# Optimization experiments

Measured on AMD Instinct MI355X. Metric: run time of the kernel, lower is better.

## Reference

```python
import math
import jax, jax.numpy as jnp
import numpy as np

B, T, C, HS = 8, 2048, 1024, 64

def setup_inputs() -> dict:
    key = jax.random.key(0)
    kx, kq, kk, kv = jax.random.split(key, 4)
    x = jax.random.normal(kx, (B, T, C), dtype=jnp.float32)
    # match nn.Linear init scale roughly: U(-1/sqrt(C), 1/sqrt(C))
    lim = 1.0 / math.sqrt(C)
    Wq = jax.random.uniform(kq, (C, HS), minval=-lim, maxval=lim, dtype=jnp.float32)
    Wk = jax.random.uniform(kk, (C, HS), minval=-lim, maxval=lim, dtype=jnp.float32)
    Wv = jax.random.uniform(kv, (C, HS), minval=-lim, maxval=lim, dtype=jnp.float32)
    return {"x": x, "Wq": Wq, "Wk": Wk, "Wv": Wv}

def reference(x, Wq, Wk, Wv):
    # NOTE: original scales by 1/sqrt(hs) where hs = x.shape[-1] = embd_size,
    # not head_size. Faithfully reproduced.
    Tlen = x.shape[1]
    scale = 1.0 / math.sqrt(x.shape[-1])
    q = jnp.einsum('btc,ch->bth', x, Wq)
    k = jnp.einsum('btc,ch->bth', x, Wk)
    v = jnp.einsum('btc,ch->bth', x, Wv)
    wei = jnp.einsum('bth,bsh->bts', q, k) * scale  # [B,T,T]
    causal = jnp.tril(jnp.ones((Tlen, Tlen), dtype=bool))
    wei = jnp.where(causal, wei, -jnp.inf)
    wei = jax.nn.softmax(wei, axis=-1)
    # dropout p=0.0 -> identity
    out = jnp.einsum('bts,bsh->bth', wei, v)  # [B,T,HS]
    return out
```

## Files before the change

### kernel.cpp

```cpp
#include <hip/hip_runtime.h>
#include <hip/hip_bf16.h>


#define T_SEQ 2048
#define C_DIM 1024
#define HS 64
#define BT 16384

typedef short s8v __attribute__((ext_vector_type(8)));
typedef float f4v __attribute__((ext_vector_type(4)));

__device__ inline unsigned short f2bf(float f) {
  union { float f; unsigned u; } a; a.f = f;
  unsigned r = a.u + 0x7fffu + ((a.u >> 16) & 1u);
  return (unsigned short)(r >> 16);
}

__device__ inline s8v cvt8(float4 v0, float4 v1) {
  union { __hip_bfloat162 h; unsigned u; } c0, c1, c2, c3;
  c0.h = __float22bfloat162_rn(make_float2(v0.x, v0.y));
  c1.h = __float22bfloat162_rn(make_float2(v0.z, v0.w));
  c2.h = __float22bfloat162_rn(make_float2(v1.x, v1.y));
  c3.h = __float22bfloat162_rn(make_float2(v1.z, v1.w));
  union { unsigned u[4]; s8v v; } r;
  r.u[0] = c0.u; r.u[1] = c1.u; r.u[2] = c2.u; r.u[3] = c3.u;
  return r.v;
}

__device__ inline void gl_lds16(const void* g, unsigned char* lds_base,
                                unsigned uniform_byte_off) {
  __builtin_amdgcn_global_load_lds(
      (const __attribute__((address_space(1))) unsigned int*)g,
      (__attribute__((address_space(3))) unsigned int*)(lds_base + uniform_byte_off),
      16, 0, 0);
}

__global__ __launch_bounds__(256) void wt_kernel(
    const float* __restrict__ Wq, const float* __restrict__ Wk,
    const float* __restrict__ Wv, unsigned short* __restrict__ wt) {
  __shared__ float tile[64][65];
  const int bid = blockIdx.x;
  const int mat = bid >> 4, kt = bid & 15;
  const float* W = (mat == 0) ? Wq : ((mat == 1) ? Wk : Wv);
  const int t = threadIdx.x;
  const int n = t & 63, kr = t >> 6;
#pragma unroll
  for (int j = 0; j < 16; ++j) {
    const int kl = j * 4 + kr;
    tile[kl][n] = W[(kt * 64 + kl) * HS + n];
  }
  __syncthreads();
  const int n2 = t >> 2, kp = t & 3;
  unsigned int* orow =
      (unsigned int*)(wt + (size_t)(mat * 64 + n2) * C_DIM + kt * 64);
#pragma unroll
  for (int i = 0; i < 8; ++i) {
    const int k0 = kp * 16 + i * 2;
    unsigned int lo = f2bf(tile[k0][n2]);
    unsigned int hi = f2bf(tile[k0 + 1][n2]);
    orow[kp * 8 + i] = lo | (hi << 16);
  }
}

__global__ __launch_bounds__(256) void qkv_kernel(
    const float* __restrict__ x, const unsigned short* __restrict__ wt,
    unsigned short* __restrict__ qws, unsigned short* __restrict__ kws,
    unsigned short* __restrict__ vtws) {
  __shared__ unsigned char abuf[2][8192];
  __shared__ unsigned char bbuf[2][24576];

  const int tid  = threadIdx.x;
  const int wv   = tid >> 6;
  const int lane = tid & 63;
  const int m    = lane & 15;
  const int quad = lane >> 4;
  const int row0 = blockIdx.x * 32;
  const int mh   = wv >> 1;
  const int ng   = (wv & 1) * 6;

  f4v acc[6];
#pragma unroll
  for (int j = 0; j < 6; ++j) acc[j] = (f4v)0.0f;

  const unsigned au = (unsigned)__builtin_amdgcn_readfirstlane(tid & 192) << 4;

  const float* agp[2];
#pragma unroll
  for (int j = 0; j < 2; ++j) {
    const int s = tid + j * 256;
    const int r = s >> 4, p = (s & 15) ^ (r & 15);
    agp[j] = x + (size_t)(row0 + r) * C_DIM + p * 4;
  }
  const unsigned short* bgp[6];
#pragma unroll
  for (int j = 0; j < 6; ++j) {
    const int s = tid + j * 256;
    const int n = s >> 3, p = (s & 7) ^ (n & 7);
    bgp[j] = wt + (size_t)n * C_DIM + p * 8;
  }

  int aoff[2][2];
#pragma unroll
  for (int c = 0; c < 2; ++c)
#pragma unroll
    for (int t = 0; t < 2; ++t)
      aoff[c][t] = (((mh * 16 + m) * 16) + ((c * 8 + 2 * quad + t) ^ m)) << 4;
  int boff[6][2];
#pragma unroll
  for (int j = 0; j < 6; ++j) {
    const int n = (ng + j) * 16 + m;
#pragma unroll
    for (int c = 0; c < 2; ++c)
      boff[j][c] = (n * 8 + ((c * 4 + quad) ^ (n & 7))) << 4;
  }

#define STAGE(buf, kk)                                                       \
  do {                                                                       \
    _Pragma("unroll") for (int j = 0; j < 2; ++j)                            \
        gl_lds16(agp[j] + (kk), abuf[buf], au + (unsigned)(j * 4096));       \
    _Pragma("unroll") for (int j = 0; j < 6; ++j)                            \
        gl_lds16(bgp[j] + (kk), bbuf[buf], au + (unsigned)(j * 4096));       \
  } while (0)

  STAGE(0, 0);
  for (int it = 0; it < 16; ++it) {
    __syncthreads();
    if (it < 15) STAGE((it + 1) & 1, (it + 1) * 64);
    const unsigned char* aB = abuf[it & 1];
    const unsigned char* bB = bbuf[it & 1];
#pragma unroll
    for (int c = 0; c < 2; ++c) {
      float4 xa = *(const float4*)(aB + aoff[c][0]);
      float4 xb = *(const float4*)(aB + aoff[c][1]);
      s8v a = cvt8(xa, xb);
#pragma unroll
      for (int j = 0; j < 6; ++j) {
        s8v b = *(const s8v*)(bB + boff[j][c]);
        acc[j] = __builtin_amdgcn_mfma_f32_16x16x32_bf16(a, b, acc[j], 0, 0, 0);
      }
    }
  }
#undef STAGE

  const float qscale = 1.4426950408889634f / 32.0f;
#pragma unroll
  for (int j = 0; j < 6; ++j) {
    const int nt = ng + j;
    const int mat = nt >> 2, ct = nt & 3;
    const int col = ct * 16 + m;
#pragma unroll
    for (int r = 0; r < 4; ++r) {
      const int row = row0 + mh * 16 + quad * 4 + r;
      const float v = acc[j][r];
      if (mat == 0) {
        qws[row * HS + col] = f2bf(v * qscale);
      } else if (mat == 1) {
        kws[row * HS + col] = f2bf(v);
      } else {
        const int bb = row >> 11, t = row & 2047;
        vtws[(bb * HS + col) * T_SEQ + t] = f2bf(v);
      }
    }
  }
}

union AttnSh {
  unsigned short p[8][16 * 72];
  float mo[8][16][64];
};

__global__ __launch_bounds__(512) void attn_kernel(
    const unsigned short* __restrict__ qws, const unsigned short* __restrict__ kws,
    const unsigned short* __restrict__ vtws, float* __restrict__ out) {
  __shared__ AttnSh sh;
  __shared__ float ml[8][16];

  const int tid  = threadIdx.x;
  const int wv   = tid >> 6;
  const int lane = tid & 63;
  const int m    = lane & 15;
  const int quad = lane >> 4;
  const int b    = blockIdx.x & 7;
  const int qt   = (T_SEQ / 16 - 1) - (blockIdx.x >> 3);
  const int r0   = qt * 16;
  const int gr0  = b * T_SEQ + r0;

  s8v aq0 = *(const s8v*)&qws[(size_t)(gr0 + m) * HS + quad * 8];
  s8v aq1 = *(const s8v*)&qws[(size_t)(gr0 + m) * HS + 32 + quad * 8];

  float li[4] = {0.f, 0.f, 0.f, 0.f};
  f4v o[4];
#pragma unroll
  for (int i = 0; i < 4; ++i) o[i] = (f4v)0.0f;

  const int nst = (r0 + 16 + 63) >> 6;
  unsigned short* pl = sh.p[wv];
  const int qrow_base = r0 + quad * 4;
  const unsigned short* kbase = kws + (size_t)b * T_SEQ * HS;
  const unsigned short* vbase = vtws + (size_t)b * HS * T_SEQ;

  for (int st = wv; st < nst; st += 8) {
    const int s0 = st * 64;

    s8v kf[4][2];
#pragma unroll
    for (int ns = 0; ns < 4; ++ns) {
      const unsigned short* kp = &kbase[(size_t)(s0 + ns * 16 + m) * HS + quad * 8];
      kf[ns][0] = *(const s8v*)kp;
      kf[ns][1] = *(const s8v*)(kp + 32);
    }
    s8v vf[4][2];
#pragma unroll
    for (int hn = 0; hn < 4; ++hn) {
      const unsigned short* vp = &vbase[(size_t)(hn * 16 + m) * T_SEQ + s0 + quad * 8];
      vf[hn][0] = *(const s8v*)vp;
      vf[hn][1] = *(const s8v*)(vp + 32);
    }

    f4v sacc[4];
#pragma unroll
    for (int ns = 0; ns < 4; ++ns) {
      f4v t = (f4v)0.0f;
      t = __builtin_amdgcn_mfma_f32_16x16x32_bf16(aq0, kf[ns][0], t, 0, 0, 0);
      t = __builtin_amdgcn_mfma_f32_16x16x32_bf16(aq1, kf[ns][1], t, 0, 0, 0);
      sacc[ns] = t;
    }

#pragma unroll
    for (int ns = 0; ns < 4; ++ns) {
      const int scol = s0 + ns * 16 + m;
#pragma unroll
      for (int r = 0; r < 4; ++r) {
        const float p = (scol > qrow_base + r) ? 0.f
                        : __builtin_amdgcn_exp2f(sacc[ns][r]);
        li[r] += p;
        pl[(quad * 4 + r) * 72 + ns * 16 + m] = f2bf(p);
      }
    }

    s8v ap0 = *(const s8v*)&pl[m * 72 + quad * 8];
    s8v ap1 = *(const s8v*)&pl[m * 72 + 32 + quad * 8];
#pragma unroll
    for (int hn = 0; hn < 4; ++hn) {
      o[hn] = __builtin_amdgcn_mfma_f32_16x16x32_bf16(ap0, vf[hn][0], o[hn], 0, 0, 0);
      o[hn] = __builtin_amdgcn_mfma_f32_16x16x32_bf16(ap1, vf[hn][1], o[hn], 0, 0, 0);
    }
  }

#pragma unroll
  for (int r = 0; r < 4; ++r) {
    float s = li[r];
    s += __shfl_xor(s, 1); s += __shfl_xor(s, 2);
    s += __shfl_xor(s, 4); s += __shfl_xor(s, 8);
    li[r] = s;
  }

  __syncthreads();

#pragma unroll
  for (int hn = 0; hn < 4; ++hn)
#pragma unroll
    for (int r = 0; r < 4; ++r)
      sh.mo[wv][quad * 4 + r][hn * 16 + m] = o[hn][r];
  if (m == 0) {
#pragma unroll
    for (int r = 0; r < 4; ++r) ml[wv][quad * 4 + r] = li[r];
  }
  __syncthreads();

  const int row = tid >> 5, cg = tid & 31;
  float ls = 0.f;
#pragma unroll
  for (int w = 0; w < 8; ++w) ls += ml[w][row];
  const float inv = 1.0f / ls;
  float rx = 0.f, ry = 0.f;
#pragma unroll
  for (int w = 0; w < 8; ++w) {
    float2 v = *(const float2*)&sh.mo[w][row][cg * 2];
    rx += v.x; ry += v.y;
  }
  float2 res; res.x = rx * inv; res.y = ry * inv;
  *(float2*)&out[(size_t)(gr0 + row) * HS + cg * 2] = res;
}

extern "C" void kernel_launch(void* const* d_in, const int* in_sizes, int n_in,
                              void* d_out, int out_size, void* d_ws, size_t ws_size,
                              hipStream_t stream) {
  const float* x  = (const float*)d_in[0];
  const float* Wq = (const float*)d_in[1];
  const float* Wk = (const float*)d_in[2];
  const float* Wv = (const float*)d_in[3];
  float* out = (float*)d_out;

  unsigned short* qws  = (unsigned short*)d_ws;
  unsigned short* kws  = qws + (size_t)BT * HS;
  unsigned short* vtws = kws + (size_t)BT * HS;
  unsigned short* wt   = vtws + (size_t)BT * HS;

  wt_kernel<<<dim3(48), dim3(256), 0, stream>>>(Wq, Wk, Wv, wt);
  qkv_kernel<<<dim3(BT / 32), dim3(256), 0, stream>>>(x, wt, qws, kws, vtws);
  attn_kernel<<<dim3(1024), dim3(512), 0, stream>>>(qws, kws, vtws, out);
}
```

Measured before the change: 153.0 us.

## Prefetch next K/V tiles in registers, interleave query-tile order, add occupancy hints

In the attention loop, the K and V fragments for the wave's next key tile are now loaded into registers before the current tile's MFMAs run, so global-load latency overlaps with compute. The query-tile mapping is changed so consecutive block indices alternate between short and long causal rows instead of running longest-first. Both kernels also gain minimum-blocks-per-CU launch-bound hints. The double-buffered fragments raise register pressure, and the occupancy hints may force spills.

```diff
diff --git a/kernel.cpp b/kernel.cpp
--- a/kernel.cpp
+++ b/kernel.cpp
@@ -62,7 +62,7 @@
   }
 }
 
-__global__ __launch_bounds__(256) void qkv_kernel(
+__global__ __launch_bounds__(256, 4) void qkv_kernel(
     const float* __restrict__ x, const unsigned short* __restrict__ wt,
     unsigned short* __restrict__ qws, unsigned short* __restrict__ kws,
     unsigned short* __restrict__ vtws) {
@@ -169,7 +169,7 @@
   float mo[8][16][64];
 };
 
-__global__ __launch_bounds__(512) void attn_kernel(
+__global__ __launch_bounds__(512, 2) void attn_kernel(
     const unsigned short* __restrict__ qws, const unsigned short* __restrict__ kws,
     const unsigned short* __restrict__ vtws, float* __restrict__ out) {
   __shared__ AttnSh sh;
@@ -181,7 +181,8 @@
   const int m    = lane & 15;
   const int quad = lane >> 4;
   const int b    = blockIdx.x & 7;
-  const int qt   = (T_SEQ / 16 - 1) - (blockIdx.x >> 3);
+  const int j    = blockIdx.x >> 3;
+  const int qt   = (j & 1) ? (127 - (j >> 1)) : (j >> 1);
   const int r0   = qt * 16;
   const int gr0  = b * T_SEQ + r0;
 
@@ -199,22 +200,33 @@
   const unsigned short* kbase = kws + (size_t)b * T_SEQ * HS;
   const unsigned short* vbase = vtws + (size_t)b * HS * T_SEQ;
 
+  s8v kf[4][2], vf[4][2];
+  {
+    const int s0c = ((wv < nst) ? wv : 0) * 64;
+#pragma unroll
+    for (int ns = 0; ns < 4; ++ns) {
+      const unsigned short* kp = &kbase[(size_t)(s0c + ns * 16 + m) * HS + quad * 8];
+      kf[ns][0] = *(const s8v*)kp;
+      kf[ns][1] = *(const s8v*)(kp + 32);
+      const unsigned short* vp = &vbase[(size_t)(ns * 16 + m) * T_SEQ + s0c + quad * 8];
+      vf[ns][0] = *(const s8v*)vp;
+      vf[ns][1] = *(const s8v*)(vp + 32);
+    }
+  }
+
   for (int st = wv; st < nst; st += 8) {
     const int s0 = st * 64;
-
-    s8v kf[4][2];
-#pragma unroll
-    for (int ns = 0; ns < 4; ++ns) {
-      const unsigned short* kp = &kbase[(size_t)(s0 + ns * 16 + m) * HS + quad * 8];
-      kf[ns][0] = *(const s8v*)kp;
-      kf[ns][1] = *(const s8v*)(kp + 32);
-    }
-    s8v vf[4][2];
-#pragma unroll
-    for (int hn = 0; hn < 4; ++hn) {
-      const unsigned short* vp = &vbase[(size_t)(hn * 16 + m) * T_SEQ + s0 + quad * 8];
-      vf[hn][0] = *(const s8v*)vp;
-      vf[hn][1] = *(const s8v*)(vp + 32);
+    const int sn = ((st + 8 < nst) ? st + 8 : st) * 64;
+
+    s8v nkf[4][2], nvf[4][2];
+#pragma unroll
+    for (int ns = 0; ns < 4; ++ns) {
+      const unsigned short* kp = &kbase[(size_t)(sn + ns * 16 + m) * HS + quad * 8];
+      nkf[ns][0] = *(const s8v*)kp;
+      nkf[ns][1] = *(const s8v*)(kp + 32);
+      const unsigned short* vp = &vbase[(size_t)(ns * 16 + m) * T_SEQ + sn + quad * 8];
+      nvf[ns][0] = *(const s8v*)vp;
+      nvf[ns][1] = *(const s8v*)(vp + 32);
     }
 
     f4v sacc[4];
@@ -244,6 +256,12 @@
     for (int hn = 0; hn < 4; ++hn) {
       o[hn] = __builtin_amdgcn_mfma_f32_16x16x32_bf16(ap0, vf[hn][0], o[hn], 0, 0, 0);
       o[hn] = __builtin_amdgcn_mfma_f32_16x16x32_bf16(ap1, vf[hn][1], o[hn], 0, 0, 0);
+    }
+
+#pragma unroll
+    for (int ns = 0; ns < 4; ++ns) {
+      kf[ns][0] = nkf[ns][0]; kf[ns][1] = nkf[ns][1];
+      vf[ns][0] = nvf[ns][0]; vf[ns][1] = nvf[ns][1];
     }
   }
 
```

New measurement: 180.6 us. 18.0% more time.

## Share K/V tiles across four query subtiles via double-buffered LDS staging

Applied to the files above, without the earlier changes.

Each attention block now covers 64 query rows (4 subtiles with 2 waves each) instead of 16. K/V tiles are staged into swizzled LDS with direct global-to-LDS loads, double-buffered so the next tile loads while the current one is consumed. Each tile is then reused by every wave, which cuts redundant global K/V reads. The cost is a block-wide barrier per tile and idle waves on alternate tiles, since each wave pair splits tiles by parity. The grid shrinks from 1024 to 256 blocks, which may reduce load balance across CUs.

```diff
diff --git a/kernel.cpp b/kernel.cpp
--- a/kernel.cpp
+++ b/kernel.cpp
@@ -165,15 +165,16 @@
 }
 
 union AttnSh {
-  unsigned short p[8][16 * 72];
-  float mo[8][16][64];
+  unsigned short p[8][16 * 76];
+  struct { float mo[4][16][64]; float ml[4][16]; } m;
 };
 
-__global__ __launch_bounds__(512) void attn_kernel(
+__global__ __launch_bounds__(512, 2) void attn_kernel(
     const unsigned short* __restrict__ qws, const unsigned short* __restrict__ kws,
     const unsigned short* __restrict__ vtws, float* __restrict__ out) {
+  __shared__ unsigned char kbuf[2][8192];
+  __shared__ unsigned char vbuf[2][8192];
   __shared__ AttnSh sh;
-  __shared__ float ml[8][16];
 
   const int tid  = threadIdx.x;
   const int wv   = tid >> 6;
@@ -181,9 +182,12 @@
   const int m    = lane & 15;
   const int quad = lane >> 4;
   const int b    = blockIdx.x & 7;
-  const int qt   = (T_SEQ / 16 - 1) - (blockIdx.x >> 3);
-  const int r0   = qt * 16;
-  const int gr0  = b * T_SEQ + r0;
+  const int qt   = 31 - (blockIdx.x >> 3);
+  const int r0   = qt * 64;
+  const int qsub = wv >> 1;
+  const int par  = wv & 1;
+  const int rw   = r0 + qsub * 16;
+  const int gr0  = b * T_SEQ + rw;
 
   s8v aq0 = *(const s8v*)&qws[(size_t)(gr0 + m) * HS + quad * 8];
   s8v aq1 = *(const s8v*)&qws[(size_t)(gr0 + m) * HS + 32 + quad * 8];
@@ -193,57 +197,73 @@
 #pragma unroll
   for (int i = 0; i < 4; ++i) o[i] = (f4v)0.0f;
 
-  const int nst = (r0 + 16 + 63) >> 6;
+  const int nst    = qt + 1;
+  const int mylast = (rw + 15) >> 6;
+  const int qrow_base = rw + quad * 4;
   unsigned short* pl = sh.p[wv];
-  const int qrow_base = r0 + quad * 4;
+
   const unsigned short* kbase = kws + (size_t)b * T_SEQ * HS;
   const unsigned short* vbase = vtws + (size_t)b * HS * T_SEQ;
 
-  for (int st = wv; st < nst; st += 8) {
-    const int s0 = st * 64;
-
-    s8v kf[4][2];
-#pragma unroll
-    for (int ns = 0; ns < 4; ++ns) {
-      const unsigned short* kp = &kbase[(size_t)(s0 + ns * 16 + m) * HS + quad * 8];
-      kf[ns][0] = *(const s8v*)kp;
-      kf[ns][1] = *(const s8v*)(kp + 32);
-    }
-    s8v vf[4][2];
-#pragma unroll
-    for (int hn = 0; hn < 4; ++hn) {
-      const unsigned short* vp = &vbase[(size_t)(hn * 16 + m) * T_SEQ + s0 + quad * 8];
-      vf[hn][0] = *(const s8v*)vp;
-      vf[hn][1] = *(const s8v*)(vp + 32);
-    }
-
-    f4v sacc[4];
-#pragma unroll
-    for (int ns = 0; ns < 4; ++ns) {
-      f4v t = (f4v)0.0f;
-      t = __builtin_amdgcn_mfma_f32_16x16x32_bf16(aq0, kf[ns][0], t, 0, 0, 0);
-      t = __builtin_amdgcn_mfma_f32_16x16x32_bf16(aq1, kf[ns][1], t, 0, 0, 0);
-      sacc[ns] = t;
-    }
-
-#pragma unroll
-    for (int ns = 0; ns < 4; ++ns) {
-      const int scol = s0 + ns * 16 + m;
-#pragma unroll
-      for (int r = 0; r < 4; ++r) {
-        const float p = (scol > qrow_base + r) ? 0.f
-                        : __builtin_amdgcn_exp2f(sacc[ns][r]);
-        li[r] += p;
-        pl[(quad * 4 + r) * 72 + ns * 16 + m] = f2bf(p);
-      }
-    }
-
-    s8v ap0 = *(const s8v*)&pl[m * 72 + quad * 8];
-    s8v ap1 = *(const s8v*)&pl[m * 72 + 32 + quad * 8];
-#pragma unroll
-    for (int hn = 0; hn < 4; ++hn) {
-      o[hn] = __builtin_amdgcn_mfma_f32_16x16x32_bf16(ap0, vf[hn][0], o[hn], 0, 0, 0);
-      o[hn] = __builtin_amdgcn_mfma_f32_16x16x32_bf16(ap1, vf[hn][1], o[hn], 0, 0, 0);
+  const int rt = tid >> 3;
+  const int pt = (tid & 7) ^ (rt & 7);
+  const unsigned au = (unsigned)__builtin_amdgcn_readfirstlane(tid & 448) << 4;
+
+  int fo[4][2];
+#pragma unroll
+  for (int ns = 0; ns < 4; ++ns)
+#pragma unroll
+    for (int c = 0; c < 2; ++c)
+      fo[ns][c] = ((ns * 16 + m) * 8 + ((c * 4 + quad) ^ (m & 7))) << 4;
+
+#define STAGEKV(buf, st)                                                     \
+  do {                                                                       \
+    const int s0_ = (st) * 64;                                               \
+    gl_lds16(kbase + (size_t)(s0_ + rt) * HS + pt * 8, kbuf[buf], au);       \
+    gl_lds16(vbase + (size_t)rt * T_SEQ + s0_ + pt * 8, vbuf[buf], au);      \
+  } while (0)
+
+  STAGEKV(0, 0);
+  for (int st = 0; st < nst; ++st) {
+    __syncthreads();
+    if (st + 1 < nst) STAGEKV((st + 1) & 1, st + 1);
+    if ((st & 1) == par && st <= mylast) {
+      const unsigned char* kB = kbuf[st & 1];
+      const unsigned char* vB = vbuf[st & 1];
+      const int s0 = st * 64;
+
+      f4v sacc[4];
+#pragma unroll
+      for (int ns = 0; ns < 4; ++ns) {
+        f4v t = (f4v)0.0f;
+        t = __builtin_amdgcn_mfma_f32_16x16x32_bf16(
+            aq0, *(const s8v*)(kB + fo[ns][0]), t, 0, 0, 0);
+        t = __builtin_amdgcn_mfma_f32_16x16x32_bf16(
+            aq1, *(const s8v*)(kB + fo[ns][1]), t, 0, 0, 0);
+        sacc[ns] = t;
+      }
+
+#pragma unroll
+      for (int ns = 0; ns < 4; ++ns) {
+        const int scol = s0 + ns * 16 + m;
+#pragma unroll
+        for (int r = 0; r < 4; ++r) {
+          const float p = (scol > qrow_base + r) ? 0.f
+                          : __builtin_amdgcn_exp2f(sacc[ns][r]);
+          li[r] += p;
+          pl[(quad * 4 + r) * 76 + ns * 16 + m] = f2bf(p);
+        }
+      }
+
+      s8v ap0 = *(const s8v*)&pl[m * 76 + quad * 8];
+      s8v ap1 = *(const s8v*)&pl[m * 76 + 32 + quad * 8];
+#pragma unroll
+      for (int hn = 0; hn < 4; ++hn) {
+        o[hn] = __builtin_amdgcn_mfma_f32_16x16x32_bf16(
+            ap0, *(const s8v*)(vB + fo[hn][0]), o[hn], 0, 0, 0);
+        o[hn] = __builtin_amdgcn_mfma_f32_16x16x32_bf16(
+            ap1, *(const s8v*)(vB + fo[hn][1]), o[hn], 0, 0, 0);
+      }
     }
   }
 
@@ -257,30 +277,30 @@
 
   __syncthreads();
 
-#pragma unroll
-  for (int hn = 0; hn < 4; ++hn)
-#pragma unroll
-    for (int r = 0; r < 4; ++r)
-      sh.mo[wv][quad * 4 + r][hn * 16 + m] = o[hn][r];
-  if (m == 0) {
-#pragma unroll
-    for (int r = 0; r < 4; ++r) ml[wv][quad * 4 + r] = li[r];
+  if (par == 1) {
+#pragma unroll
+    for (int hn = 0; hn < 4; ++hn)
+#pragma unroll
+      for (int r = 0; r < 4; ++r)
+        sh.m.mo[qsub][quad * 4 + r][hn * 16 + m] = o[hn][r];
+    if (m == 0) {
+#pragma unroll
+      for (int r = 0; r < 4; ++r) sh.m.ml[qsub][quad * 4 + r] = li[r];
+    }
   }
   __syncthreads();
-
-  const int row = tid >> 5, cg = tid & 31;
-  float ls = 0.f;
-#pragma unroll
-  for (int w = 0; w < 8; ++w) ls += ml[w][row];
-  const float inv = 1.0f / ls;
-  float rx = 0.f, ry = 0.f;
-#pragma unroll
-  for (int w = 0; w < 8; ++w) {
-    float2 v = *(const float2*)&sh.mo[w][row][cg * 2];
-    rx += v.x; ry += v.y;
-  }
-  float2 res; res.x = rx * inv; res.y = ry * inv;
-  *(float2*)&out[(size_t)(gr0 + row) * HS + cg * 2] = res;
+  if (par == 0) {
+#pragma unroll
+    for (int r = 0; r < 4; ++r) {
+      const int row = quad * 4 + r;
+      const float inv = 1.0f / (li[r] + sh.m.ml[qsub][row]);
+#pragma unroll
+      for (int hn = 0; hn < 4; ++hn) {
+        const float v = o[hn][r] + sh.m.mo[qsub][row][hn * 16 + m];
+        out[(size_t)(gr0 + row) * HS + hn * 16 + m] = v * inv;
+      }
+    }
+  }
 }
 
 extern "C" void kernel_launch(void* const* d_in, const int* in_sizes, int n_in,
@@ -299,5 +319,5 @@
 
   wt_kernel<<<dim3(48), dim3(256), 0, stream>>>(Wq, Wk, Wv, wt);
   qkv_kernel<<<dim3(BT / 32), dim3(256), 0, stream>>>(x, wt, qws, kws, vtws);
-  attn_kernel<<<dim3(1024), dim3(512), 0, stream>>>(qws, kws, vtws, out);
-}
+  attn_kernel<<<dim3(256), dim3(512), 0, stream>>>(qws, kws, vtws, out);
+}
```

Result: slower. 158.5 us (+3.6%).
